# Kernel tuning notes

Hardware: AMD Instinct MI355X
Metric: run time of the kernel (lower is better)

The kernel has to match this reference:

```python
import jax, jax.numpy as jnp
import numpy as np

BETA = 0.95
THR = 1.0
NUM_STEPS = 25
NUM_IN, NUM_HID, NUM_OUT = 9, 100, 2
BATCH = 65536


def _heaviside(x):
    return (x > 0).astype(x.dtype)


def setup_inputs() -> dict:
    key = jax.random.key(0)
    ks = jax.random.split(key, 5)
    x = jax.random.normal(ks[0], (BATCH, NUM_IN), dtype=jnp.float32)
    # nn.Linear default init: U(-1/sqrt(fan_in), 1/sqrt(fan_in))
    b1lim = 1.0 / np.sqrt(NUM_IN)
    b2lim = 1.0 / np.sqrt(NUM_HID)
    W1 = jax.random.uniform(ks[1], (NUM_HID, NUM_IN), jnp.float32, -b1lim, b1lim)
    b1 = jax.random.uniform(ks[2], (NUM_HID,), jnp.float32, -b1lim, b1lim)
    W2 = jax.random.uniform(ks[3], (NUM_OUT, NUM_HID), jnp.float32, -b2lim, b2lim)
    b2 = jax.random.uniform(ks[4], (NUM_OUT,), jnp.float32, -b2lim, b2lim)
    return {"x": x, "W1": W1, "b1": b1, "W2": W2, "b2": b2}


def reference(x, W1, b1, W2, b2):
    # cur1 = fc1(x) is identical every step (x is static) -> hoist out of loop
    cur1 = x @ W1.T + b1                     # [B, 100]
    mem1 = jnp.zeros((x.shape[0], NUM_HID), x.dtype)
    mem2 = jnp.zeros((x.shape[0], NUM_OUT), x.dtype)

    def step(carry, _):
        mem1, mem2 = carry
        # snntorch Leaky, reset_mechanism='subtract': reset from PREVIOUS mem
        reset1 = _heaviside(mem1 - THR)
        mem1 = BETA * mem1 + cur1 - reset1 * THR
        spk1 = _heaviside(mem1 - THR)        # [B, 100]
        cur2 = spk1 @ W2.T + b2              # [B, 2]
        reset2 = _heaviside(mem2 - THR)
        mem2 = BETA * mem2 + cur2 - reset2 * THR
        return (mem1, mem2), mem2

    (_, _), mem2_rec = jax.lax.scan(step, (mem1, mem2), None, length=NUM_STEPS)
    return mem2_rec                          # [25, B, 2]
```

## Files before the change

kernel.cpp:

```cpp
#include <hip/hip_runtime.h>

#define BATCH  65536
#define NIN    9
#define NHID   100
#define TSTEPS 25
#define CHUNK  5
#define EPS    3e-5f

typedef float v2f __attribute__((ext_vector_type(2)));

__global__ __launch_bounds__(256) void snn_kernel(
    const float* __restrict__ x,  const float* __restrict__ W1,
    const float* __restrict__ b1, const float* __restrict__ W2,
    const float* __restrict__ b2, float* __restrict__ out)
{
    __shared__ float sx[64 * NIN];
    __shared__ v2f   sacc[2][4][CHUNK][64];

    const int tid  = threadIdx.x;
    const int lane = tid & 63;
    const int wq   = __builtin_amdgcn_readfirstlane(tid >> 6);
    const int b0   = blockIdx.x * 64;

    for (int i = tid; i < 64 * NIN; i += 256) sx[i] = x[(size_t)b0 * NIN + i];
    __syncthreads();

    float xv[NIN];
#pragma unroll
    for (int i = 0; i < NIN; ++i) xv[i] = sx[lane * NIN + i];

    float a0[TSTEPS], a1[TSTEPS];
#pragma unroll
    for (int t = 0; t < TSTEPS; ++t) { a0[t] = 0.f; a1[t] = 0.f; }

    const int h0 = wq * 25;
#pragma unroll 1
    for (int j = 0; j < 25; ++j) {
        const int h = h0 + j;
        float c32 = 0.f;
#pragma unroll
        for (int i = 0; i < NIN; ++i) c32 = fmaf(W1[h * NIN + i], xv[i], c32);
        c32 += b1[h];
        const float k  = c32 - 0.05f;
        const float k1 = c32 - 1.05f;
        const float w0 = W2[h], w1 = W2[NHID + h];

        float u = -1.0f, ming = 1e30f;
        bool  s = false;
#pragma unroll
        for (int t = 0; t < TSTEPS; ++t) {
            u = fmaf(0.95f, u, s ? k1 : k);
            s = (u > 0.0f);
            ming = fminf(ming, fabsf(u));
            float d = s ? 1.f : 0.f;
            a0[t] = fmaf(d, w0, a0[t]);
            a1[t] = fmaf(d, w1, a1[t]);
        }

        if (__any(ming < EPS)) {
            double c64 = 0.0;
#pragma unroll
            for (int i = 0; i < NIN; ++i)
                c64 += (double)W1[h * NIN + i] * (double)xv[i];
            c64 += (double)b1[h];
            const double c1 = c64 - 1.0;

            double md = 0.0;  bool sd = false;
            float  ur = -1.0f; bool sr = false;
#pragma unroll
            for (int t = 0; t < TSTEPS; ++t) {
                ur = fmaf(0.95f, ur, sr ? k1 : k);
                sr = (ur > 0.0f);
                md = 0.95 * md + (sd ? c1 : c64);
                sd = (md > 1.0);
                if (sr != sd) {
                    float sg = sd ? 1.f : -1.f;
                    a0[t] = fmaf(sg, w0, a0[t]);
                    a1[t] = fmaf(sg, w1, a1[t]);
                }
            }
        }
    }

    double m20 = 0.0, m21 = 0.0;
    double bb0 = (double)b2[0], bb1 = (double)b2[1];

#pragma unroll
    for (int k = 0; k < TSTEPS / CHUNK; ++k) {
#pragma unroll
        for (int u = 0; u < CHUNK; ++u)
            sacc[k & 1][wq][u][lane] = (v2f){a0[k * CHUNK + u], a1[k * CHUNK + u]};
        __syncthreads();
        if (wq == 0) {
#pragma unroll
            for (int u = 0; u < CHUNK; ++u) {
                const int t = k * CHUNK + u;
                v2f q0 = sacc[k & 1][0][u][lane];
                v2f q1 = sacc[k & 1][1][u][lane];
                v2f q2 = sacc[k & 1][2][u][lane];
                v2f q3 = sacc[k & 1][3][u][lane];
                v2f sum = (q0 + q1) + (q2 + q3);
                double r0 = (m20 > 1.0) ? 1.0 : 0.0;
                double r1 = (m21 > 1.0) ? 1.0 : 0.0;
                m20 = 0.95 * m20 + ((double)sum[0] + bb0) - r0;
                m21 = 0.95 * m21 + ((double)sum[1] + bb1) - r1;
                *(float2*)(out + ((size_t)t * BATCH + b0 + lane) * 2) =
                    make_float2((float)m20, (float)m21);
            }
        }
    }
}

extern "C" void kernel_launch(void* const* d_in, const int* in_sizes, int n_in,
                              void* d_out, int out_size, void* d_ws, size_t ws_size,
                              hipStream_t stream) {
    const float* x  = (const float*)d_in[0];
    const float* W1 = (const float*)d_in[1];
    const float* b1 = (const float*)d_in[2];
    const float* W2 = (const float*)d_in[3];
    const float* b2 = (const float*)d_in[4];
    float* out = (float*)d_out;

    dim3 grid(BATCH / 64), block(256);
    hipLaunchKernelGGL(snn_kernel, grid, block, 0, stream, x, W1, b1, W2, b2, out);
}
```

Before: 98.21 us.

## Pack per-neuron spike trains into bitmasks in LDS and defer fc2 accumulation

```diff
diff --git a/kernel.cpp b/kernel.cpp
--- a/kernel.cpp
+++ b/kernel.cpp
@@ -15,6 +15,7 @@
     const float* __restrict__ b2, float* __restrict__ out)
 {
     __shared__ float sx[64 * NIN];
+    __shared__ unsigned int sbits[4][25][64];
     __shared__ v2f   sacc[2][4][CHUNK][64];
 
     const int tid  = threadIdx.x;
@@ -29,12 +30,9 @@
 #pragma unroll
     for (int i = 0; i < NIN; ++i) xv[i] = sx[lane * NIN + i];
 
-    float a0[TSTEPS], a1[TSTEPS];
-#pragma unroll
-    for (int t = 0; t < TSTEPS; ++t) { a0[t] = 0.f; a1[t] = 0.f; }
+    const int h0 = wq * 25;
 
-    const int h0 = wq * 25;
-#pragma unroll 1
+    unsigned int badmask = 0;
     for (int j = 0; j < 25; ++j) {
         const int h = h0 + j;
         float c32 = 0.f;
@@ -43,21 +41,31 @@
         c32 += b1[h];
         const float k  = c32 - 0.05f;
         const float k1 = c32 - 1.05f;
-        const float w0 = W2[h], w1 = W2[NHID + h];
 
         float u = -1.0f, ming = 1e30f;
         bool  s = false;
+        unsigned int mask = 0;
 #pragma unroll
         for (int t = 0; t < TSTEPS; ++t) {
             u = fmaf(0.95f, u, s ? k1 : k);
             s = (u > 0.0f);
+            mask = (mask << 1) | (s ? 1u : 0u);
             ming = fminf(ming, fabsf(u));
-            float d = s ? 1.f : 0.f;
-            a0[t] = fmaf(d, w0, a0[t]);
-            a1[t] = fmaf(d, w1, a1[t]);
         }
+        sbits[wq][j][lane] = mask;
+        badmask |= __any(ming < EPS) ? (1u << j) : 0u;
+    }
 
-        if (__any(ming < EPS)) {
+    if (badmask) {
+        for (int j = 0; j < 25; ++j) {
+            if (!((badmask >> j) & 1u)) continue;
+            const int h = h0 + j;
+            float c32 = 0.f;
+#pragma unroll
+            for (int i = 0; i < NIN; ++i) c32 = fmaf(W1[h * NIN + i], xv[i], c32);
+            c32 += b1[h];
+            const float k  = c32 - 0.05f;
+            const float k1 = c32 - 1.05f;
             double c64 = 0.0;
 #pragma unroll
             for (int i = 0; i < NIN; ++i)
@@ -65,40 +73,54 @@
             c64 += (double)b1[h];
             const double c1 = c64 - 1.0;
 
-            double md = 0.0;  bool sd = false;
             float  ur = -1.0f; bool sr = false;
+            double md = 0.0;   bool sd = false;
+            unsigned int fix = 0;
 #pragma unroll
             for (int t = 0; t < TSTEPS; ++t) {
                 ur = fmaf(0.95f, ur, sr ? k1 : k);
                 sr = (ur > 0.0f);
                 md = 0.95 * md + (sd ? c1 : c64);
                 sd = (md > 1.0);
-                if (sr != sd) {
-                    float sg = sd ? 1.f : -1.f;
-                    a0[t] = fmaf(sg, w0, a0[t]);
-                    a1[t] = fmaf(sg, w1, a1[t]);
-                }
+                fix = (fix << 1) | ((sr != sd) ? 1u : 0u);
             }
+            sbits[wq][j][lane] ^= fix;
         }
     }
 
     double m20 = 0.0, m21 = 0.0;
-    double bb0 = (double)b2[0], bb1 = (double)b2[1];
+    const double bb0 = (double)b2[0], bb1 = (double)b2[1];
+
+#pragma unroll 1
+    for (int c = 0; c < TSTEPS / CHUNK; ++c) {
+        float acc0[CHUNK], acc1[CHUNK];
+#pragma unroll
+        for (int i = 0; i < CHUNK; ++i) { acc0[i] = 0.f; acc1[i] = 0.f; }
 
 #pragma unroll
-    for (int k = 0; k < TSTEPS / CHUNK; ++k) {
+        for (int j = 0; j < 25; ++j) {
+            const unsigned int bits = sbits[wq][j][lane];
+            const float w0 = W2[h0 + j], w1 = W2[NHID + h0 + j];
+#pragma unroll
+            for (int i = 0; i < CHUNK; ++i) {
+                const float d = (float)((bits >> (24 - (CHUNK * c + i))) & 1u);
+                acc0[i] = fmaf(d, w0, acc0[i]);
+                acc1[i] = fmaf(d, w1, acc1[i]);
+            }
+        }
+
 #pragma unroll
         for (int u = 0; u < CHUNK; ++u)
-            sacc[k & 1][wq][u][lane] = (v2f){a0[k * CHUNK + u], a1[k * CHUNK + u]};
+            sacc[c & 1][wq][u][lane] = (v2f){acc0[u], acc1[u]};
         __syncthreads();
         if (wq == 0) {
 #pragma unroll
             for (int u = 0; u < CHUNK; ++u) {
-                const int t = k * CHUNK + u;
-                v2f q0 = sacc[k & 1][0][u][lane];
-                v2f q1 = sacc[k & 1][1][u][lane];
-                v2f q2 = sacc[k & 1][2][u][lane];
-                v2f q3 = sacc[k & 1][3][u][lane];
+                const int t = c * CHUNK + u;
+                v2f q0 = sacc[c & 1][0][u][lane];
+                v2f q1 = sacc[c & 1][1][u][lane];
+                v2f q2 = sacc[c & 1][2][u][lane];
+                v2f q3 = sacc[c & 1][3][u][lane];
                 v2f sum = (q0 + q1) + (q2 + q3);
                 double r0 = (m20 > 1.0) ? 1.0 : 0.0;
                 double r1 = (m21 > 1.0) ? 1.0 : 0.0;
```

New measurement: 112.7 us. 1.15x slower.

## Split timestep accumulation into two passes to cut register pressure

Applied to the files above, without the earlier changes.

```diff
diff --git a/kernel.cpp b/kernel.cpp
--- a/kernel.cpp
+++ b/kernel.cpp
@@ -9,7 +9,7 @@
 
 typedef float v2f __attribute__((ext_vector_type(2)));
 
-__global__ __launch_bounds__(256) void snn_kernel(
+__global__ __launch_bounds__(256, 4) void snn_kernel(
     const float* __restrict__ x,  const float* __restrict__ W1,
     const float* __restrict__ b1, const float* __restrict__ W2,
     const float* __restrict__ b2, float* __restrict__ out)
@@ -29,83 +29,167 @@
 #pragma unroll
     for (int i = 0; i < NIN; ++i) xv[i] = sx[lane * NIN + i];
 
-    float a0[TSTEPS], a1[TSTEPS];
-#pragma unroll
-    for (int t = 0; t < TSTEPS; ++t) { a0[t] = 0.f; a1[t] = 0.f; }
-
     const int h0 = wq * 25;
+    unsigned int badmask = 0;
+
+    double m20 = 0.0, m21 = 0.0;
+    const double bb0 = (double)b2[0], bb1 = (double)b2[1];
+
+    {
+        float a0[15], a1[15];
+#pragma unroll
+        for (int t = 0; t < 15; ++t) { a0[t] = 0.f; a1[t] = 0.f; }
+
 #pragma unroll 1
-    for (int j = 0; j < 25; ++j) {
-        const int h = h0 + j;
-        float c32 = 0.f;
-#pragma unroll
-        for (int i = 0; i < NIN; ++i) c32 = fmaf(W1[h * NIN + i], xv[i], c32);
-        c32 += b1[h];
-        const float k  = c32 - 0.05f;
-        const float k1 = c32 - 1.05f;
-        const float w0 = W2[h], w1 = W2[NHID + h];
-
-        float u = -1.0f, ming = 1e30f;
-        bool  s = false;
-#pragma unroll
-        for (int t = 0; t < TSTEPS; ++t) {
-            u = fmaf(0.95f, u, s ? k1 : k);
-            s = (u > 0.0f);
-            ming = fminf(ming, fabsf(u));
-            float d = s ? 1.f : 0.f;
-            a0[t] = fmaf(d, w0, a0[t]);
-            a1[t] = fmaf(d, w1, a1[t]);
-        }
-
-        if (__any(ming < EPS)) {
-            double c64 = 0.0;
-#pragma unroll
-            for (int i = 0; i < NIN; ++i)
-                c64 += (double)W1[h * NIN + i] * (double)xv[i];
-            c64 += (double)b1[h];
-            const double c1 = c64 - 1.0;
-
-            double md = 0.0;  bool sd = false;
-            float  ur = -1.0f; bool sr = false;
+        for (int j = 0; j < 25; ++j) {
+            const int h = h0 + j;
+            float c32 = 0.f;
+#pragma unroll
+            for (int i = 0; i < NIN; ++i) c32 = fmaf(W1[h*NIN+i], xv[i], c32);
+            c32 += b1[h];
+            const float k  = c32 - 0.05f;
+            const float k1 = c32 - 1.05f;
+            const float w0 = W2[h], w1 = W2[NHID + h];
+
+            float u = -1.0f, ming = 1e30f;
+            bool  s = false;
 #pragma unroll
             for (int t = 0; t < TSTEPS; ++t) {
-                ur = fmaf(0.95f, ur, sr ? k1 : k);
-                sr = (ur > 0.0f);
-                md = 0.95 * md + (sd ? c1 : c64);
-                sd = (md > 1.0);
-                if (sr != sd) {
-                    float sg = sd ? 1.f : -1.f;
-                    a0[t] = fmaf(sg, w0, a0[t]);
-                    a1[t] = fmaf(sg, w1, a1[t]);
+                u = fmaf(0.95f, u, s ? k1 : k);
+                s = (u > 0.0f);
+                ming = fminf(ming, fabsf(u));
+                if (t < 15) {
+                    const float d = s ? 1.f : 0.f;
+                    a0[t] = fmaf(d, w0, a0[t]);
+                    a1[t] = fmaf(d, w1, a1[t]);
+                }
+            }
+            if (__any(ming < EPS)) {
+                badmask |= (1u << j);
+                double c64 = 0.0;
+#pragma unroll
+                for (int i = 0; i < NIN; ++i)
+                    c64 += (double)W1[h*NIN+i] * (double)xv[i];
+                c64 += (double)b1[h];
+                const double c1 = c64 - 1.0;
+                float  ur = -1.0f; bool sr = false;
+                double md = 0.0;   bool sd = false;
+#pragma unroll
+                for (int t = 0; t < TSTEPS; ++t) {
+                    ur = fmaf(0.95f, ur, sr ? k1 : k);
+                    sr = (ur > 0.0f);
+                    md = 0.95 * md + (sd ? c1 : c64);
+                    sd = (md > 1.0);
+                    if (t < 15 && sr != sd) {
+                        const float sg = sd ? 1.f : -1.f;
+                        a0[t] = fmaf(sg, w0, a0[t]);
+                        a1[t] = fmaf(sg, w1, a1[t]);
+                    }
+                }
+            }
+        }
+#pragma unroll
+        for (int kc = 0; kc < 3; ++kc) {
+#pragma unroll
+            for (int u2 = 0; u2 < CHUNK; ++u2)
+                sacc[kc & 1][wq][u2][lane] =
+                    (v2f){a0[kc*CHUNK + u2], a1[kc*CHUNK + u2]};
+            __syncthreads();
+            if (wq == 0) {
+#pragma unroll
+                for (int u2 = 0; u2 < CHUNK; ++u2) {
+                    const int t = kc*CHUNK + u2;
+                    v2f q0 = sacc[kc & 1][0][u2][lane];
+                    v2f q1 = sacc[kc & 1][1][u2][lane];
+                    v2f q2 = sacc[kc & 1][2][u2][lane];
+                    v2f q3 = sacc[kc & 1][3][u2][lane];
+                    v2f sum = (q0 + q1) + (q2 + q3);
+                    double r0 = (m20 > 1.0) ? 1.0 : 0.0;
+                    double r1 = (m21 > 1.0) ? 1.0 : 0.0;
+                    m20 = 0.95*m20 + ((double)sum[0] + bb0) - r0;
+                    m21 = 0.95*m21 + ((double)sum[1] + bb1) - r1;
+                    *(float2*)(out + ((size_t)t*BATCH + b0 + lane)*2) =
+                        make_float2((float)m20, (float)m21);
                 }
             }
         }
     }
 
-    double m20 = 0.0, m21 = 0.0;
-    double bb0 = (double)b2[0], bb1 = (double)b2[1];
-
-#pragma unroll
-    for (int k = 0; k < TSTEPS / CHUNK; ++k) {
-#pragma unroll
-        for (int u = 0; u < CHUNK; ++u)
-            sacc[k & 1][wq][u][lane] = (v2f){a0[k * CHUNK + u], a1[k * CHUNK + u]};
-        __syncthreads();
-        if (wq == 0) {
-#pragma unroll
-            for (int u = 0; u < CHUNK; ++u) {
-                const int t = k * CHUNK + u;
-                v2f q0 = sacc[k & 1][0][u][lane];
-                v2f q1 = sacc[k & 1][1][u][lane];
-                v2f q2 = sacc[k & 1][2][u][lane];
-                v2f q3 = sacc[k & 1][3][u][lane];
-                v2f sum = (q0 + q1) + (q2 + q3);
-                double r0 = (m20 > 1.0) ? 1.0 : 0.0;
-                double r1 = (m21 > 1.0) ? 1.0 : 0.0;
-                m20 = 0.95 * m20 + ((double)sum[0] + bb0) - r0;
-                m21 = 0.95 * m21 + ((double)sum[1] + bb1) - r1;
-                *(float2*)(out + ((size_t)t * BATCH + b0 + lane) * 2) =
-                    make_float2((float)m20, (float)m21);
+    {
+        float a0[10], a1[10];
+#pragma unroll
+        for (int t = 0; t < 10; ++t) { a0[t] = 0.f; a1[t] = 0.f; }
+
+#pragma unroll 1
+        for (int j = 0; j < 25; ++j) {
+            const int h = h0 + j;
+            float c32 = 0.f;
+#pragma unroll
+            for (int i = 0; i < NIN; ++i) c32 = fmaf(W1[h*NIN+i], xv[i], c32);
+            c32 += b1[h];
+            const float k  = c32 - 0.05f;
+            const float k1 = c32 - 1.05f;
+            const float w0 = W2[h], w1 = W2[NHID + h];
+
+            float u = -1.0f;
+            bool  s = false;
+#pragma unroll
+            for (int t = 0; t < TSTEPS; ++t) {
+                u = fmaf(0.95f, u, s ? k1 : k);
+                s = (u > 0.0f);
+                if (t >= 15) {
+                    const float d = s ? 1.f : 0.f;
+                    a0[t-15] = fmaf(d, w0, a0[t-15]);
+                    a1[t-15] = fmaf(d, w1, a1[t-15]);
+                }
+            }
+            if ((badmask >> j) & 1u) {
+                double c64 = 0.0;
+#pragma unroll
+                for (int i = 0; i < NIN; ++i)
+                    c64 += (double)W1[h*NIN+i] * (double)xv[i];
+                c64 += (double)b1[h];
+                const double c1 = c64 - 1.0;
+                float  ur = -1.0f; bool sr = false;
+                double md = 0.0;   bool sd = false;
+#pragma unroll
+                for (int t = 0; t < TSTEPS; ++t) {
+                    ur = fmaf(0.95f, ur, sr ? k1 : k);
+                    sr = (ur > 0.0f);
+                    md = 0.95 * md + (sd ? c1 : c64);
+                    sd = (md > 1.0);
+                    if (t >= 15 && sr != sd) {
+                        const float sg = sd ? 1.f : -1.f;
+                        a0[t-15] = fmaf(sg, w0, a0[t-15]);
+                        a1[t-15] = fmaf(sg, w1, a1[t-15]);
+                    }
+                }
+            }
+        }
+#pragma unroll
+        for (int kc = 0; kc < 2; ++kc) {
+            const int kg = 3 + kc;
+#pragma unroll
+            for (int u2 = 0; u2 < CHUNK; ++u2)
+                sacc[kg & 1][wq][u2][lane] =
+                    (v2f){a0[kc*CHUNK + u2], a1[kc*CHUNK + u2]};
+            __syncthreads();
+            if (wq == 0) {
+#pragma unroll
+                for (int u2 = 0; u2 < CHUNK; ++u2) {
+                    const int t = 15 + kc*CHUNK + u2;
+                    v2f q0 = sacc[kg & 1][0][u2][lane];
+                    v2f q1 = sacc[kg & 1][1][u2][lane];
+                    v2f q2 = sacc[kg & 1][2][u2][lane];
+                    v2f q3 = sacc[kg & 1][3][u2][lane];
+                    v2f sum = (q0 + q1) + (q2 + q3);
+                    double r0 = (m20 > 1.0) ? 1.0 : 0.0;
+                    double r1 = (m21 > 1.0) ? 1.0 : 0.0;
+                    m20 = 0.95*m20 + ((double)sum[0] + bb0) - r0;
+                    m21 = 0.95*m21 + ((double)sum[1] + bb1) - r1;
+                    *(float2*)(out + ((size_t)t*BATCH + b0 + lane)*2) =
+                        make_float2((float)m20, (float)m21);
+                }
             }
         }
     }
```

Result: slower. 113.2 us (+15.2%).
